# Kernel tuning notes

Measured on AMD Instinct MI355X. Metric: run time of the kernel, lower is better.

## Reference

```python
import jax, jax.numpy as jnp
import numpy as np

BLOCK_H = 32  # block_h from init
BLOCK_W = 32  # block_w from init


def _block_pool(mask, bh, bw):
    # mask: [H, S, S] int -> block mask [H, S//bh, S//bw] bool
    # Equivalent to the grouped Conv2d with all-ones kernel, stride=(bh,bw), then >0.
    H, S1, S2 = mask.shape
    m = mask.reshape(H, S1 // bh, bh, S2 // bw, bw).astype(jnp.float32)
    return m.sum(axis=(2, 4)) > 0


def _expand_block_mask(bm, bh, bw):
    # bm: [H, Nb_r, Nb_c] bool -> element mask [H, S, S] bool
    H, nr, nc = bm.shape
    e = jnp.broadcast_to(bm[:, :, None, :, None], (H, nr, bh, nc, bw))
    return e.reshape(H, nr * bh, nc * bw)


def setup_inputs() -> dict:
    key = jax.random.key(0)
    kq, kk, kv, km = jax.random.split(key, 4)
    Z, H, S, D = 1, 16, 2048, 64
    query = jax.random.normal(kq, (Z, H, S, D), dtype=jnp.float32)
    key_t = jax.random.normal(kk, (Z, H, S, D), dtype=jnp.float32)
    value = jax.random.normal(kv, (Z, H, S, D), dtype=jnp.float32)
    mask = jax.random.randint(km, (H, S, S), 0, 2, dtype=jnp.int32)
    return {"query": query, "key": key_t, "value": value, "mask": mask}


def reference(query, key, value, mask):
    # Dense equivalent of: sdd QK^T on layout blocks -> blocksparse causal
    # softmax (scale=1.0) -> dsd AV. Rows with no active blocks yield zeros,
    # matching the blocksparse representation (absent blocks contribute 0).
    H, S, _ = mask.shape
    bm = _block_pool(mask, BLOCK_H, BLOCK_W)              # [H, Nb, Nb]
    elem = _expand_block_mask(bm, BLOCK_H, BLOCK_W)       # [H, S, S]
    causal = jnp.tril(jnp.ones((S, S), dtype=bool))       # is_causal=True
    full = elem & causal                                  # [H, S, S]
    scale = 1.0                                           # scale=1.0 in forward

    scores = jnp.einsum('zhqd,zhkd->zhqk', query, key) * scale
    neg = jnp.asarray(-1e30, dtype=scores.dtype)
    scores = jnp.where(full[None], scores, neg)
    probs = jax.nn.softmax(scores, axis=-1)
    row_valid = jnp.any(full, axis=-1)                    # [H, S]
    probs = jnp.where(row_valid[None, :, :, None], probs, 0.0)
    out = jnp.einsum('zhqk,zhkd->zhqd', probs, value)
    return out
```

## Files before the change

kernel.cpp:

```cpp
#include <hip/hip_runtime.h>
#include <stdint.h>


#define HH 16
#define SS 2048
#define DD 64

using f32x4  = __attribute__((ext_vector_type(4))) float;
using s16x8  = __attribute__((ext_vector_type(8))) short;
using s16x4  = __attribute__((ext_vector_type(4))) short;
using bf16x8 = __attribute__((ext_vector_type(8))) __bf16;

#define AS1 __attribute__((address_space(1)))
#define AS3 __attribute__((address_space(3)))

__device__ __forceinline__ unsigned short f2bf(float f) {
  unsigned u = __builtin_bit_cast(unsigned, f);
  u += 0x7fffu + ((u >> 16) & 1u);
  return (unsigned short)(u >> 16);
}
__device__ __forceinline__ float bf2f(unsigned short u) {
  return __builtin_bit_cast(float, ((unsigned)u) << 16);
}

__global__ __launch_bounds__(256) void prep_kernel(
    const int* __restrict__ mask, const float* __restrict__ K,
    const float* __restrict__ V, unsigned char* __restrict__ bmask,
    unsigned short* __restrict__ Khi, unsigned short* __restrict__ Klo,
    unsigned short* __restrict__ Vtb) {
  __shared__ float tile[64][65];
  const int wg = blockIdx.x;
  const int t  = threadIdx.x;
  if (wg < 256) {
    const int tid = wg * 256 + t;
    {
      const int h = tid >> 12, br = (tid >> 6) & 63, bc = tid & 63;
      const int4* p = (const int4*)(mask + ((size_t)(h * SS + br * 32) * SS + bc * 32));
      int acc = 0;
#pragma unroll
      for (int i = 0; i < 8; ++i) { int4 v = p[i]; acc |= v.x | v.y | v.z | v.w; }
      if (acc == 0) {
        for (int r = 1; r < 32; ++r) {
          const int4* q2 = (const int4*)(mask + ((size_t)(h * SS + br * 32 + r) * SS + bc * 32));
          int a2 = 0;
#pragma unroll
          for (int i = 0; i < 8; ++i) { int4 v = q2[i]; a2 |= v.x | v.y | v.z | v.w; }
          acc |= a2;
          if (acc) break;
        }
      }
      bmask[tid] = acc != 0 ? 1 : 0;
    }
    {
      const float4* K4 = (const float4*)K;
      ushort4* Kh4 = (ushort4*)Khi;
      ushort4* Kl4 = (ushort4*)Klo;
#pragma unroll
      for (int i = 0; i < 8; ++i) {
        float4 v = K4[(size_t)i * 65536 + tid];
        ushort4 hi, lo;
        hi.x = f2bf(v.x); lo.x = f2bf(v.x - bf2f(hi.x));
        hi.y = f2bf(v.y); lo.y = f2bf(v.y - bf2f(hi.y));
        hi.z = f2bf(v.z); lo.z = f2bf(v.z - bf2f(hi.z));
        hi.w = f2bf(v.w); lo.w = f2bf(v.w - bf2f(hi.w));
        Kh4[(size_t)i * 65536 + tid] = hi;
        Kl4[(size_t)i * 65536 + tid] = lo;
      }
    }
  } else {
    const int w2 = wg - 256;
    const int h = w2 >> 5, kt = w2 & 31;
    const float4* V4 = (const float4*)V;
#pragma unroll
    for (int j2 = 0; j2 < 4; ++j2) {
      int fi = t + j2 * 256;
      int row = fi >> 4, c4 = (fi & 15) * 4;
      float4 v = V4[(size_t)(h * SS + kt * 64 + row) * 16 + (fi & 15)];
      tile[row][c4] = v.x; tile[row][c4+1] = v.y; tile[row][c4+2] = v.z; tile[row][c4+3] = v.w;
    }
    __syncthreads();
    const int d = t >> 2, ks = (t & 3) * 16;
#pragma unroll
    for (int c = 0; c < 4; ++c) {
      ushort4 o;
      o.x = f2bf(tile[ks + c*4 + 0][d]);
      o.y = f2bf(tile[ks + c*4 + 1][d]);
      o.z = f2bf(tile[ks + c*4 + 2][d]);
      o.w = f2bf(tile[ks + c*4 + 3][d]);
      ((ushort4*)Vtb)[((size_t)(h * 64 + d) * SS + kt * 64 + ks + c*4) >> 2] = o;
    }
  }
}

__global__ __launch_bounds__(256) void attn_kernel(
    const float* __restrict__ Q, const unsigned char* __restrict__ bmask,
    const unsigned short* __restrict__ Khi, const unsigned short* __restrict__ Klo,
    const unsigned short* __restrict__ Vtb, float* __restrict__ O) {
  const int id = blockIdx.x;
  const int h  = id & 15;
  const int j  = id >> 4;
  const int qb = (j < 16) ? j : 47 - j;

  const int t    = threadIdx.x;
  const int wave = t >> 6, lane = t & 63;
  const int n16  = lane & 15, quad = lane >> 4;

  __shared__ __align__(16) short ldsKV[24576];
  __shared__ __align__(16) short ldsP[4][1088];

  const int qi0 = qb * 64 + wave * 16;
  s16x8 qhi[2], qlo[2];
  {
    const float* qp = Q + ((size_t)(h * SS + qi0 + n16)) * DD + quad * 8;
#pragma unroll
    for (int kc = 0; kc < 2; ++kc) {
      float4 a = *(const float4*)(qp + kc * 32);
      float4 b = *(const float4*)(qp + kc * 32 + 4);
      float x[8] = {a.x, a.y, a.z, a.w, b.x, b.y, b.z, b.w};
      s16x8 fh, fl;
#pragma unroll
      for (int e = 0; e < 8; ++e) {
        unsigned short hi = f2bf(x[e]);
        fh[e] = (short)hi;
        fl[e] = (short)f2bf(x[e] - bf2f(hi));
      }
      qhi[kc] = fh; qlo[kc] = fl;
    }
  }

  const int qbr = qb * 2 + (wave >> 1);
  const unsigned long long bmw = __ballot(bmask[(h << 12) + (qbr << 6) + lane] != 0);

  float m_i[4], l_i[4];
  f32x4 oa[4];
#pragma unroll
  for (int r = 0; r < 4; ++r) { m_i[r] = -__builtin_inff(); l_i[r] = 0.f; }
#pragma unroll
  for (int db = 0; db < 4; ++db) oa[db] = f32x4{0.f, 0.f, 0.f, 0.f};

  auto stage = [&](int kt, int buf) {
    short* kh = ldsKV + buf * 12288;
    short* kl = kh + 4096;
    short* vd = kh + 8192;
#pragma unroll
    for (int i = 0; i < 2; ++i) {
      int slot = i * 256 + t;
      int row  = slot >> 3;
      int c8   = (slot & 7) ^ (row & 7);
      size_t koff = ((size_t)(h * SS + kt * 64 + row)) * DD + c8 * 8;
      __builtin_amdgcn_global_load_lds((const AS1 void*)(Khi + koff),
                                       (AS3 void*)(kh + slot * 8), 16, 0, 0);
      __builtin_amdgcn_global_load_lds((const AS1 void*)(Klo + koff),
                                       (AS3 void*)(kl + slot * 8), 16, 0, 0);
      const unsigned short* gv = Vtb + ((size_t)(h * 64 + row)) * SS + kt * 64 + c8 * 8;
      __builtin_amdgcn_global_load_lds((const AS1 void*)gv,
                                       (AS3 void*)(vd + slot * 8), 16, 0, 0);
    }
  };

  stage(0, 0);
  for (int kt = 0; kt <= qb; ++kt) {
    const int buf = kt & 1;
    __syncthreads();
    if (kt < qb) stage(kt + 1, buf ^ 1);

    const short* khb = ldsKV + buf * 12288;
    const short* klb = khb + 4096;
    const short* vbase = khb + 8192;

    f32x4 S[4];
#pragma unroll
    for (int nb = 0; nb < 4; ++nb) S[nb] = f32x4{0.f, 0.f, 0.f, 0.f};
#pragma unroll
    for (int kc = 0; kc < 2; ++kc) {
      bf16x8 ah = __builtin_bit_cast(bf16x8, qhi[kc]);
      bf16x8 al8 = __builtin_bit_cast(bf16x8, qlo[kc]);
#pragma unroll
      for (int nb = 0; nb < 4; ++nb) {
        int row = nb * 16 + n16;
        int pc  = (kc * 4 + quad) ^ (row & 7);
        bf16x8 kh = __builtin_bit_cast(bf16x8, *(const s16x8*)(khb + row * 64 + pc * 8));
        bf16x8 kl = __builtin_bit_cast(bf16x8, *(const s16x8*)(klb + row * 64 + pc * 8));
        S[nb] = __builtin_amdgcn_mfma_f32_16x16x32_bf16(ah, kh, S[nb], 0, 0, 0);
        S[nb] = __builtin_amdgcn_mfma_f32_16x16x32_bf16(al8, kh, S[nb], 0, 0, 0);
        S[nb] = __builtin_amdgcn_mfma_f32_16x16x32_bf16(ah, kl, S[nb], 0, 0, 0);
      }
    }

    const int b0 = (int)((bmw >> (kt * 2)) & 1ull);
    const int b1 = (int)((bmw >> (kt * 2 + 1)) & 1ull);
#pragma unroll
    for (int nb = 0; nb < 4; ++nb) {
      int kj = kt * 64 + nb * 16 + n16;
      int bb = (nb < 2) ? b0 : b1;
#pragma unroll
      for (int r = 0; r < 4; ++r) {
        int qi = qi0 + quad * 4 + r;
        bool ok = (kj <= qi) && (bb != 0);
        S[nb][r] = ok ? S[nb][r] : -__builtin_inff();
      }
    }

#pragma unroll
    for (int r = 0; r < 4; ++r) {
      float mx = fmaxf(fmaxf(S[0][r], S[1][r]), fmaxf(S[2][r], S[3][r]));
      mx = fmaxf(mx, __shfl_xor(mx, 1));
      mx = fmaxf(mx, __shfl_xor(mx, 2));
      mx = fmaxf(mx, __shfl_xor(mx, 4));
      mx = fmaxf(mx, __shfl_xor(mx, 8));
      float mn = fmaxf(m_i[r], mx);
      bool valid = mn > -1e37f;
      float al = valid ? __expf(m_i[r] - mn) : 1.f;
      if (valid) m_i[r] = mn;
      float rsum = 0.f;
#pragma unroll
      for (int nb = 0; nb < 4; ++nb) {
        float p = valid ? __expf(S[nb][r] - mn) : 0.f;
        unsigned short pq = f2bf(p);
        ldsP[wave][(quad * 4 + r) * 68 + nb * 16 + n16] = (short)pq;
        rsum += bf2f(pq);
      }
      rsum += __shfl_xor(rsum, 1); rsum += __shfl_xor(rsum, 2);
      rsum += __shfl_xor(rsum, 4); rsum += __shfl_xor(rsum, 8);
      l_i[r] = l_i[r] * al + rsum;
#pragma unroll
      for (int db = 0; db < 4; ++db) oa[db][r] *= al;
    }

#pragma unroll
    for (int kc = 0; kc < 2; ++kc) {
      const short* pp = &ldsP[wave][n16 * 68 + kc * 32 + quad * 8];
      s16x4 x = *(const s16x4*)pp;
      s16x4 y = *(const s16x4*)(pp + 4);
      s16x8 pf8 = {x[0], x[1], x[2], x[3], y[0], y[1], y[2], y[3]};
      bf16x8 ap = __builtin_bit_cast(bf16x8, pf8);
#pragma unroll
      for (int db = 0; db < 4; ++db) {
        int row = db * 16 + n16;
        int pc  = (kc * 4 + quad) ^ (n16 & 7);
        s16x8 vv = *(const s16x8*)(vbase + row * 64 + pc * 8);
        oa[db] = __builtin_amdgcn_mfma_f32_16x16x32_bf16(
            ap, __builtin_bit_cast(bf16x8, vv), oa[db], 0, 0, 0);
      }
    }
  }

  float* op = O + ((size_t)(h * SS + qi0)) * DD;
#pragma unroll
  for (int r = 0; r < 4; ++r) {
    int qrow = quad * 4 + r;
    float inv = l_i[r] > 0.f ? 1.f / l_i[r] : 0.f;
#pragma unroll
    for (int db = 0; db < 4; ++db) {
      op[(size_t)qrow * DD + db * 16 + n16] = oa[db][r] * inv;
    }
  }
}

extern "C" void kernel_launch(void* const* d_in, const int* in_sizes, int n_in,
                              void* d_out, int out_size, void* d_ws, size_t ws_size,
                              hipStream_t stream) {
  const float* Q   = (const float*)d_in[0];
  const float* K   = (const float*)d_in[1];
  const float* V   = (const float*)d_in[2];
  const int* mask  = (const int*)d_in[3];
  float* out       = (float*)d_out;

  unsigned char* bmask = (unsigned char*)d_ws;
  unsigned short* Khi  = (unsigned short*)((char*)d_ws + 65536);
  unsigned short* Klo  = (unsigned short*)((char*)d_ws + 65536 + 4194304);
  unsigned short* Vtb  = (unsigned short*)((char*)d_ws + 65536 + 2 * 4194304);

  prep_kernel<<<768, 256, 0, stream>>>(mask, K, V, bmask, Khi, Klo, Vtb);
  attn_kernel<<<512, 256, 0, stream>>>(Q, bmask, Khi, Klo, Vtb, out);
}
```

Baseline: 383.4 us.

## Pair causal query blocks per workgroup and use DPP row reductions

Each workgroup now handles query block p and then 31-p in one continuous 33-step key loop, so every workgroup does equal causal work. The launch drops from 512 to 256 blocks, and the K/V staging pipeline keeps running across the switch between the two query blocks. Row max and sum reductions switch from shfl_xor to DPP row operations. Masking is skipped for fully active non-diagonal tiles. The launch bound is set to one block per SM. The risk is that 256 workgroups may underfill a 256-CU GPU, with only one block per CU and less latency hiding.

```diff
diff --git a/kernel.cpp b/kernel.cpp
--- a/kernel.cpp
+++ b/kernel.cpp
@@ -21,6 +21,28 @@
 }
 __device__ __forceinline__ float bf2f(unsigned short u) {
   return __builtin_bit_cast(float, ((unsigned)u) << 16);
+}
+
+template <int CTRL>
+__device__ __forceinline__ float dpp_step(float x) {
+  int y = __builtin_amdgcn_update_dpp(__builtin_bit_cast(int, x),
+                                      __builtin_bit_cast(int, x),
+                                      CTRL, 0xF, 0xF, false);
+  return __builtin_bit_cast(float, y);
+}
+__device__ __forceinline__ float row16_max(float x) {
+  x = fmaxf(x, dpp_step<0xB1>(x));
+  x = fmaxf(x, dpp_step<0x4E>(x));
+  x = fmaxf(x, dpp_step<0x141>(x));
+  x = fmaxf(x, dpp_step<0x140>(x));
+  return x;
+}
+__device__ __forceinline__ float row16_sum(float x) {
+  x += dpp_step<0xB1>(x);
+  x += dpp_step<0x4E>(x);
+  x += dpp_step<0x141>(x);
+  x += dpp_step<0x140>(x);
+  return x;
 }
 
 __global__ __launch_bounds__(256) void prep_kernel(
@@ -92,14 +114,13 @@
   }
 }
 
-__global__ __launch_bounds__(256) void attn_kernel(
+__global__ __launch_bounds__(256, 1) void attn_kernel(
     const float* __restrict__ Q, const unsigned char* __restrict__ bmask,
     const unsigned short* __restrict__ Khi, const unsigned short* __restrict__ Klo,
     const unsigned short* __restrict__ Vtb, float* __restrict__ O) {
   const int id = blockIdx.x;
   const int h  = id & 15;
-  const int j  = id >> 4;
-  const int qb = (j < 16) ? j : 47 - j;
+  const int p  = id >> 4;
 
   const int t    = threadIdx.x;
   const int wave = t >> 6, lane = t & 63;
@@ -108,10 +129,34 @@
   __shared__ __align__(16) short ldsKV[24576];
   __shared__ __align__(16) short ldsP[4][1088];
 
-  const int qi0 = qb * 64 + wave * 16;
+  const unsigned short* gk[2]; const unsigned short* gl[2]; const unsigned short* gv[2];
+  int lofs[2];
+#pragma unroll
+  for (int i = 0; i < 2; ++i) {
+    int slot = i * 256 + t;
+    int row  = slot >> 3;
+    int c8   = (slot & 7) ^ (row & 7);
+    lofs[i] = slot * 8;
+    gk[i] = Khi + (size_t)h * SS * DD + row * DD + c8 * 8;
+    gl[i] = Klo + (size_t)h * SS * DD + row * DD + c8 * 8;
+    gv[i] = Vtb + ((size_t)(h * 64 + row)) * SS + c8 * 8;
+  }
+  auto stage = [&](int kt, int buf) {
+    short* kb = ldsKV + buf * 12288;
+#pragma unroll
+    for (int i = 0; i < 2; ++i) {
+      __builtin_amdgcn_global_load_lds((const AS1 void*)(gk[i] + kt * 4096),
+                                       (AS3 void*)(kb + lofs[i]), 16, 0, 0);
+      __builtin_amdgcn_global_load_lds((const AS1 void*)(gl[i] + kt * 4096),
+                                       (AS3 void*)(kb + 4096 + lofs[i]), 16, 0, 0);
+      __builtin_amdgcn_global_load_lds((const AS1 void*)(gv[i] + kt * 64),
+                                       (AS3 void*)(kb + 8192 + lofs[i]), 16, 0, 0);
+    }
+  };
+
   s16x8 qhi[2], qlo[2];
-  {
-    const float* qp = Q + ((size_t)(h * SS + qi0 + n16)) * DD + quad * 8;
+  auto load_q = [&](int qb) {
+    const float* qp = Q + ((size_t)(h * SS + qb * 64 + wave * 16 + n16)) * DD + quad * 8;
 #pragma unroll
     for (int kc = 0; kc < 2; ++kc) {
       float4 a = *(const float4*)(qp + kc * 32);
@@ -126,45 +171,54 @@
       }
       qhi[kc] = fh; qlo[kc] = fl;
     }
-  }
-
-  const int qbr = qb * 2 + (wave >> 1);
-  const unsigned long long bmw = __ballot(bmask[(h << 12) + (qbr << 6) + lane] != 0);
+  };
+  auto load_bmw = [&](int qb) {
+    int qbr = qb * 2 + (wave >> 1);
+    return __ballot(bmask[(h << 12) + (qbr << 6) + lane] != 0);
+  };
 
   float m_i[4], l_i[4];
   f32x4 oa[4];
-#pragma unroll
-  for (int r = 0; r < 4; ++r) { m_i[r] = -__builtin_inff(); l_i[r] = 0.f; }
-#pragma unroll
-  for (int db = 0; db < 4; ++db) oa[db] = f32x4{0.f, 0.f, 0.f, 0.f};
-
-  auto stage = [&](int kt, int buf) {
-    short* kh = ldsKV + buf * 12288;
-    short* kl = kh + 4096;
-    short* vd = kh + 8192;
-#pragma unroll
-    for (int i = 0; i < 2; ++i) {
-      int slot = i * 256 + t;
-      int row  = slot >> 3;
-      int c8   = (slot & 7) ^ (row & 7);
-      size_t koff = ((size_t)(h * SS + kt * 64 + row)) * DD + c8 * 8;
-      __builtin_amdgcn_global_load_lds((const AS1 void*)(Khi + koff),
-                                       (AS3 void*)(kh + slot * 8), 16, 0, 0);
-      __builtin_amdgcn_global_load_lds((const AS1 void*)(Klo + koff),
-                                       (AS3 void*)(kl + slot * 8), 16, 0, 0);
-      const unsigned short* gv = Vtb + ((size_t)(h * 64 + row)) * SS + kt * 64 + c8 * 8;
-      __builtin_amdgcn_global_load_lds((const AS1 void*)gv,
-                                       (AS3 void*)(vd + slot * 8), 16, 0, 0);
-    }
-  };
-
+  auto reset_state = [&]() {
+#pragma unroll
+    for (int r = 0; r < 4; ++r) { m_i[r] = -__builtin_inff(); l_i[r] = 0.f; }
+#pragma unroll
+    for (int db = 0; db < 4; ++db) oa[db] = f32x4{0.f, 0.f, 0.f, 0.f};
+  };
+  auto store_o = [&](int qb) {
+    float* op = O + ((size_t)(h * SS + qb * 64 + wave * 16)) * DD;
+#pragma unroll
+    for (int r = 0; r < 4; ++r) {
+      int qrow = quad * 4 + r;
+      float inv = l_i[r] > 0.f ? 1.f / l_i[r] : 0.f;
+#pragma unroll
+      for (int db = 0; db < 4; ++db) {
+        op[(size_t)qrow * DD + db * 16 + n16] = oa[db][r] * inv;
+      }
+    }
+  };
+
+  int qb = p, qi0 = p * 64 + wave * 16;
+  load_q(p);
+  unsigned long long bmw = load_bmw(p);
+  reset_state();
   stage(0, 0);
-  for (int kt = 0; kt <= qb; ++kt) {
-    const int buf = kt & 1;
+
+  for (int s = 0; s < 33; ++s) {
     __syncthreads();
-    if (kt < qb) stage(kt + 1, buf ^ 1);
-
-    const short* khb = ldsKV + buf * 12288;
+    const int kt = (s <= p) ? s : s - p - 1;
+    if (s < 32) {
+      int s2 = s + 1;
+      stage((s2 <= p) ? s2 : s2 - p - 1, s2 & 1);
+    }
+    if (s == p + 1) {
+      store_o(p);
+      qb = 31 - p; qi0 = qb * 64 + wave * 16;
+      load_q(qb); bmw = load_bmw(qb);
+      reset_state();
+    }
+
+    const short* khb = ldsKV + (s & 1) * 12288;
     const short* klb = khb + 4096;
     const short* vbase = khb + 8192;
 
@@ -189,25 +243,24 @@
 
     const int b0 = (int)((bmw >> (kt * 2)) & 1ull);
     const int b1 = (int)((bmw >> (kt * 2 + 1)) & 1ull);
-#pragma unroll
-    for (int nb = 0; nb < 4; ++nb) {
-      int kj = kt * 64 + nb * 16 + n16;
-      int bb = (nb < 2) ? b0 : b1;
-#pragma unroll
-      for (int r = 0; r < 4; ++r) {
-        int qi = qi0 + quad * 4 + r;
-        bool ok = (kj <= qi) && (bb != 0);
-        S[nb][r] = ok ? S[nb][r] : -__builtin_inff();
+    if ((kt == qb) | !(b0 & b1)) {
+#pragma unroll
+      for (int nb = 0; nb < 4; ++nb) {
+        int kj = kt * 64 + nb * 16 + n16;
+        int bb = (nb < 2) ? b0 : b1;
+#pragma unroll
+        for (int r = 0; r < 4; ++r) {
+          int qi = qi0 + quad * 4 + r;
+          bool ok = (kj <= qi) && (bb != 0);
+          S[nb][r] = ok ? S[nb][r] : -__builtin_inff();
+        }
       }
     }
 
 #pragma unroll
     for (int r = 0; r < 4; ++r) {
       float mx = fmaxf(fmaxf(S[0][r], S[1][r]), fmaxf(S[2][r], S[3][r]));
-      mx = fmaxf(mx, __shfl_xor(mx, 1));
-      mx = fmaxf(mx, __shfl_xor(mx, 2));
-      mx = fmaxf(mx, __shfl_xor(mx, 4));
-      mx = fmaxf(mx, __shfl_xor(mx, 8));
+      mx = row16_max(mx);
       float mn = fmaxf(m_i[r], mx);
       bool valid = mn > -1e37f;
       float al = valid ? __expf(m_i[r] - mn) : 1.f;
@@ -215,16 +268,14 @@
       float rsum = 0.f;
 #pragma unroll
       for (int nb = 0; nb < 4; ++nb) {
-        float p = valid ? __expf(S[nb][r] - mn) : 0.f;
-        unsigned short pq = f2bf(p);
+        float pv = valid ? __expf(S[nb][r] - mn) : 0.f;
+        unsigned short pq = f2bf(pv);
         ldsP[wave][(quad * 4 + r) * 68 + nb * 16 + n16] = (short)pq;
         rsum += bf2f(pq);
       }
-      rsum += __shfl_xor(rsum, 1); rsum += __shfl_xor(rsum, 2);
-      rsum += __shfl_xor(rsum, 4); rsum += __shfl_xor(rsum, 8);
+      rsum = row16_sum(rsum);
       l_i[r] = l_i[r] * al + rsum;
-#pragma unroll
-      for (int db = 0; db < 4; ++db) oa[db][r] *= al;
+      oa[0][r] *= al; oa[1][r] *= al; oa[2][r] *= al; oa[3][r] *= al;
     }
 
 #pragma unroll
@@ -245,16 +296,7 @@
     }
   }
 
-  float* op = O + ((size_t)(h * SS + qi0)) * DD;
-#pragma unroll
-  for (int r = 0; r < 4; ++r) {
-    int qrow = quad * 4 + r;
-    float inv = l_i[r] > 0.f ? 1.f / l_i[r] : 0.f;
-#pragma unroll
-    for (int db = 0; db < 4; ++db) {
-      op[(size_t)qrow * DD + db * 16 + n16] = oa[db][r] * inv;
-    }
-  }
+  store_o(31 - p);
 }
 
 extern "C" void kernel_launch(void* const* d_in, const int* in_sizes, int n_in,
@@ -272,5 +314,5 @@
   unsigned short* Vtb  = (unsigned short*)((char*)d_ws + 65536 + 2 * 4194304);
 
   prep_kernel<<<768, 256, 0, stream>>>(mask, K, V, bmask, Khi, Klo, Vtb);
-  attn_kernel<<<512, 256, 0, stream>>>(Q, bmask, Khi, Klo, Vtb, out);
-}
+  attn_kernel<<<256, 256, 0, stream>>>(Q, bmask, Khi, Klo, Vtb, out);
+}
```

Measured after the change: 367.7 us. -4.1%, faster.
